# Kernel tuning notes

Measured on AMD Instinct MI355X. Metric: run time of the kernel, lower is better.

## Reference

```python
import jax, jax.numpy as jnp
import numpy as np

EPS = 1e-5

def _layer_norm(x, w, b):
    mu = jnp.mean(x, axis=-1, keepdims=True)
    var = jnp.mean(jnp.square(x - mu), axis=-1, keepdims=True)
    return (x - mu) * jax.lax.rsqrt(var + EPS) * w + b

def setup_inputs() -> dict:
    B, N, C, H, CH = 1, 256, 128, 4, 32
    key = jax.random.key(0)
    ks = jax.random.split(key, 8)
    s = 0.02
    return {
        "z": jax.random.normal(ks[0], (B, N, N, C), dtype=jnp.float32),
        "pair_mask": jnp.ones((B, N, N), dtype=jnp.float32),
        "ln_w": jnp.ones((C,), dtype=jnp.float32),
        "ln_b": jnp.zeros((C,), dtype=jnp.float32),
        "Wq": jax.random.normal(ks[1], (H * CH, C), dtype=jnp.float32) * s,
        "Wk": jax.random.normal(ks[2], (H * CH, C), dtype=jnp.float32) * s,
        "Wv": jax.random.normal(ks[3], (H * CH, C), dtype=jnp.float32) * s,
        "Wb": jax.random.normal(ks[4], (H, C), dtype=jnp.float32) * s,
        "Wg": jax.random.normal(ks[5], (H * CH, C), dtype=jnp.float32) * s,
        "bg": jnp.zeros((H * CH,), dtype=jnp.float32),
        "Wo": jax.random.normal(ks[6], (C, H * CH), dtype=jnp.float32) * s,
        "bo": jnp.zeros((C,), dtype=jnp.float32),
    }

def reference(z, pair_mask, ln_w, ln_b, Wq, Wk, Wv, Wb, Wg, bg, Wo, bo):
    B, I, J, C = z.shape
    H = Wb.shape[0]
    CH = Wq.shape[0] // H
    zn = _layer_norm(z, ln_w, ln_b)                      # (B,I,J,C)
    q = (zn @ Wq.T).reshape(B, I, J, H, CH)
    k = (zn @ Wk.T).reshape(B, I, J, H, CH)
    v = (zn @ Wv.T).reshape(B, I, J, H, CH)
    bias = zn @ Wb.T                                     # (B,I,J,H) -> per-head pair bias
    g = jax.nn.sigmoid(zn @ Wg.T + bg)                   # (B,I,J,H*CH)
    scale = 1.0 / jnp.sqrt(jnp.asarray(CH, z.dtype))
    # logits[b,h,i,j,k] = q_ij . k_ik / sqrt(CH) + bias[b,h,j,k]
    logits = jnp.einsum('bijhd,bikhd->bhijk', q, k) * scale
    logits = logits + jnp.transpose(bias, (0, 3, 1, 2))[:, :, None, :, :]
    # pair mask: (B,i,j,k) outer product, True = attend
    mask2d = (pair_mask[..., :, None] * pair_mask[..., None, :]) > 0.5
    logits = jnp.where(mask2d[:, None], logits, jnp.asarray(-1e9, logits.dtype))
    probs = jax.nn.softmax(logits, axis=-1)
    o = jnp.einsum('bhijk,bikhd->bijhd', probs, v).reshape(B, I, J, H * CH)
    o = g * o
    return o @ Wo.T + bo
```

## Files before the change

### kernel.cpp

```cpp
#include <hip/hip_runtime.h>
#include <hip/hip_bf16.h>

#define ATT_SCALE 0.17677669529663687f
#define LOG2E     1.4426950408889634f

typedef __attribute__((ext_vector_type(8))) short short8v;
typedef __attribute__((ext_vector_type(4))) float f32x4;
typedef __attribute__((ext_vector_type(16))) float f32x16;

__device__ __forceinline__ short f2bf(float f) {
    unsigned u = __builtin_bit_cast(unsigned, f);
    u = u + 0x7fffu + ((u >> 16) & 1u);
    return (short)(u >> 16);
}
__device__ __forceinline__ float bf2f(short s) {
    unsigned u = ((unsigned)(unsigned short)s) << 16;
    return __builtin_bit_cast(float, u);
}
__device__ __forceinline__ unsigned pk2(float lo, float hi) {
    return (unsigned)(unsigned short)f2bf(lo) |
           ((unsigned)(unsigned short)f2bf(hi) << 16);
}
__device__ __forceinline__ float lo16f(unsigned w) {
    return __builtin_bit_cast(float, w << 16);
}
__device__ __forceinline__ float hi16f(unsigned w) {
    return __builtin_bit_cast(float, w & 0xffff0000u);
}
__device__ __forceinline__ float exp2i(float x) {
    float r;
    asm("v_exp_f32 %0, %1" : "=v"(r) : "v"(x));
    return r;
}
__device__ __forceinline__ unsigned short f2h(float f) {
    _Float16 h = (_Float16)f;
    return __builtin_bit_cast(unsigned short, h);
}
__device__ __forceinline__ float h2f(unsigned short u) {
    return (float)__builtin_bit_cast(_Float16, u);
}

__global__ __launch_bounds__(256) void k_wprep(
    const float* __restrict__ Wq, const float* __restrict__ Wk,
    const float* __restrict__ Wv, const float* __restrict__ Wg,
    const float* __restrict__ Wb, const float* __restrict__ Wo,
    unsigned short* __restrict__ wbf, unsigned short* __restrict__ wbbf,
    unsigned short* __restrict__ wohi, unsigned short* __restrict__ wolo)
{
    int idx = blockIdx.x * 256 + threadIdx.x;
    if (idx < 65536) {
        int m = idx >> 14, e = idx & 16383;
        float v;
        if (m == 0)      v = Wq[e] * (ATT_SCALE * LOG2E);
        else if (m == 1) v = Wk[e];
        else if (m == 2) v = Wv[e];
        else             v = Wg[e];
        wbf[idx] = (unsigned short)f2bf(v);
    } else if (idx < 66048) {
        int e = idx - 65536;
        wbbf[e] = (unsigned short)f2bf(Wb[e]);
    } else if (idx < 82432) {
        int e = idx - 66048;
        float w = Wo[e];
        short hv = f2bf(w);
        wohi[e] = (unsigned short)hv;
        wolo[e] = (unsigned short)f2bf(w - bf2f(hv));
    }
}

__global__ __launch_bounds__(256, 4) void k_lnproj(
    const float* __restrict__ z, const float* __restrict__ lnw,
    const float* __restrict__ lnb,
    const unsigned short* __restrict__ wbf, const unsigned short* __restrict__ wbbf,
    const float* __restrict__ bg,
    unsigned short* __restrict__ q_o, unsigned short* __restrict__ k_o,
    unsigned short* __restrict__ vt_o, unsigned short* __restrict__ g_o,
    unsigned* __restrict__ bTP)
{
    __shared__ __align__(16) short zn[64][136];
    __shared__ __align__(16) short wstg[4][32][40];

    const int tid  = threadIdx.x;
    const int lane = tid & 63;
    const int wave = tid >> 6;
    const int l15  = lane & 15;
    const int g    = lane >> 4;
    const int wc   = wave;
    const long p0  = (long)blockIdx.x * 64;
    const int xq   = (int)(p0 >> 8);
    const int y0   = (int)(p0 & 255);

    {
        const int r = tid >> 2, q4 = tid & 3;
        const float* zrow = z + (p0 + r) * 128 + q4 * 32;
        float4 xv[8];
        float s1 = 0.f, s2 = 0.f;
#pragma unroll
        for (int m = 0; m < 8; ++m) {
            xv[m] = *(const float4*)(zrow + m * 4);
            s1 += xv[m].x + xv[m].y + xv[m].z + xv[m].w;
            s2 += xv[m].x * xv[m].x + xv[m].y * xv[m].y +
                  xv[m].z * xv[m].z + xv[m].w * xv[m].w;
        }
        s1 += __shfl_xor(s1, 1); s2 += __shfl_xor(s2, 1);
        s1 += __shfl_xor(s1, 2); s2 += __shfl_xor(s2, 2);
        float mu  = s1 * 0.0078125f;
        float inv = rsqrtf(s2 * 0.0078125f - mu * mu + 1e-5f);
#pragma unroll
        for (int mm = 0; mm < 4; ++mm) {
            float4 a = xv[2 * mm], b = xv[2 * mm + 1];
            const float* wp = lnw + q4 * 32 + mm * 8;
            const float* bp = lnb + q4 * 32 + mm * 8;
            float4 w0 = *(const float4*)wp, w1 = *(const float4*)(wp + 4);
            float4 b0 = *(const float4*)bp, b1 = *(const float4*)(bp + 4);
            uint4 uu;
            uu.x = pk2((a.x - mu) * inv * w0.x + b0.x, (a.y - mu) * inv * w0.y + b0.y);
            uu.y = pk2((a.z - mu) * inv * w0.z + b0.z, (a.w - mu) * inv * w0.w + b0.w);
            uu.z = pk2((b.x - mu) * inv * w1.x + b1.x, (b.y - mu) * inv * w1.y + b1.y);
            uu.w = pk2((b.z - mu) * inv * w1.z + b1.z, (b.w - mu) * inv * w1.w + b1.w);
            *(uint4*)&zn[r][q4 * 32 + mm * 8] = uu;
        }
    }
    __syncthreads();

    if (wc == 0) {
        const unsigned short* wbp = wbbf + (l15 & 3) * 128;
        short8v wb[4];
#pragma unroll
        for (int ks = 0; ks < 4; ++ks)
            wb[ks] = *(const short8v*)(wbp + ks * 32 + g * 8);
        f32x4 bacc[4];
#pragma unroll
        for (int rt = 0; rt < 4; ++rt) bacc[rt] = (f32x4){0.f, 0.f, 0.f, 0.f};
#pragma unroll
        for (int ks = 0; ks < 4; ++ks)
#pragma unroll
            for (int rt = 0; rt < 4; ++rt) {
                short8v a = *(const short8v*)&zn[rt * 16 + l15][ks * 32 + g * 8];
                bacc[rt] = __builtin_amdgcn_mfma_f32_16x16x32_bf16(a, wb[ks], bacc[rt], 0, 0, 0);
            }
        if (l15 < 4) {
#pragma unroll
            for (int rt = 0; rt < 4; ++rt) {
                int kb = y0 + rt * 16 + g * 4;
                unsigned w0 = pk2(bacc[rt][0] * LOG2E, bacc[rt][1] * LOG2E);
                unsigned w1 = pk2(bacc[rt][2] * LOG2E, bacc[rt][3] * LOG2E);
                bTP[l15 * 32768 + (kb >> 1) * 256 + xq]       = w0;
                bTP[l15 * 32768 + ((kb >> 1) + 1) * 256 + xq] = w1;
            }
        }
    }

    for (int wsel = 0; wsel < 4; ++wsel) {
        const unsigned short* __restrict__ W = wbf + wsel * 16384;
        f32x4 acc[4][2];
#pragma unroll
        for (int rt = 0; rt < 4; ++rt) {
            acc[rt][0] = (f32x4){0.f, 0.f, 0.f, 0.f};
            acc[rt][1] = (f32x4){0.f, 0.f, 0.f, 0.f};
        }
#pragma unroll
        for (int ks = 0; ks < 4; ++ks) {
            short8v b0 = *(const short8v*)(W + (wc * 32 + l15) * 128 + ks * 32 + g * 8);
            short8v b1 = *(const short8v*)(W + (wc * 32 + 16 + l15) * 128 + ks * 32 + g * 8);
#pragma unroll
            for (int rt = 0; rt < 4; ++rt) {
                short8v a = *(const short8v*)&zn[rt * 16 + l15][ks * 32 + g * 8];
                acc[rt][0] = __builtin_amdgcn_mfma_f32_16x16x32_bf16(a, b0, acc[rt][0], 0, 0, 0);
                acc[rt][1] = __builtin_amdgcn_mfma_f32_16x16x32_bf16(a, b1, acc[rt][1], 0, 0, 0);
            }
        }

        if (wsel == 3) {
#pragma unroll
            for (int pair = 0; pair < 2; ++pair) {
#pragma unroll
                for (int rt2 = 0; rt2 < 2; ++rt2)
#pragma unroll
                    for (int ct = 0; ct < 2; ++ct) {
                        float bgc = bg[wc * 32 + ct * 16 + l15];
#pragma unroll
                        for (int r = 0; r < 4; ++r) {
                            float val = acc[pair * 2 + rt2][ct][r] + bgc;
                            wstg[wave][rt2 * 16 + g * 4 + r][ct * 16 + l15] =
                                (short)f2h(1.0f / (1.0f + __expf(-val)));
                        }
                    }
#pragma unroll
                for (int ps = 0; ps < 2; ++ps) {
                    int idx = ps * 64 + lane;
                    int lr = idx >> 2, ch = (idx & 3) * 8;
                    short8v vv = *(const short8v*)&wstg[wave][lr][ch];
                    *(short8v*)(g_o + ((long)wc * 65536 + p0 + pair * 32 + lr) * 32 + ch) = vv;
                }
            }
        } else if (wsel == 2) {
#pragma unroll
            for (int pair = 0; pair < 2; ++pair) {
#pragma unroll
                for (int rt2 = 0; rt2 < 2; ++rt2)
#pragma unroll
                    for (int ct = 0; ct < 2; ++ct) {
                        uint2 pw;
                        pw.x = pk2(acc[pair * 2 + rt2][ct][0], acc[pair * 2 + rt2][ct][1]);
                        pw.y = pk2(acc[pair * 2 + rt2][ct][2], acc[pair * 2 + rt2][ct][3]);
                        *(uint2*)&wstg[wave][ct * 16 + l15][rt2 * 16 + g * 4] = pw;
                    }
#pragma unroll
                for (int e = 0; e < 4; ++e) {
                    int idx = e * 64 + lane;
                    int d = idx >> 3, k4 = idx & 7;
                    int k4p = ((k4 & 1) << 1) | ((k4 >> 1) & 1) | (k4 & 4);
                    short4 sv = *(const short4*)&wstg[wave][d][k4 * 4];
                    *(short4*)(vt_o + (((long)wc * 256 + xq) * 32 + d) * 256 +
                               y0 + pair * 32 + k4p * 4) = sv;
                }
            }
        } else {
            unsigned short* __restrict__ O = (wsel == 0) ? q_o : k_o;
#pragma unroll
            for (int pair = 0; pair < 2; ++pair) {
#pragma unroll
                for (int rt2 = 0; rt2 < 2; ++rt2)
#pragma unroll
                    for (int ct = 0; ct < 2; ++ct)
#pragma unroll
                        for (int r = 0; r < 4; ++r)
                            wstg[wave][rt2 * 16 + g * 4 + r][ct * 16 + l15] =
                                f2bf(acc[pair * 2 + rt2][ct][r]);
#pragma unroll
                for (int ps = 0; ps < 2; ++ps) {
                    int idx = ps * 64 + lane;
                    int lr = idx >> 2, ch = (idx & 3) * 8;
                    short8v vv = *(const short8v*)&wstg[wave][lr][ch];
                    *(short8v*)(O + ((long)wc * 65536 + p0 + pair * 32 + lr) * 32 + ch) = vv;
                }
            }
        }
    }
}

__global__ __launch_bounds__(256, 2) void k_attn_mfma(
    const unsigned short* __restrict__ q_ws, const unsigned short* __restrict__ k_ws,
    const unsigned short* __restrict__ vt_ws, const unsigned short* __restrict__ g_ws,
    const unsigned* __restrict__ bTP, const float* __restrict__ pm,
    unsigned short* __restrict__ ob)
{
    __shared__ __align__(16) short Ksh[256][40];
    __shared__ __align__(16) short VTsh[32][264];
    __shared__ float pmsh[256];

    const int tid  = threadIdx.x;
    const int lane = tid & 63;
    const int wave = tid >> 6;
    const int l31  = lane & 31;
    const int hi   = lane >> 5;
    const int bid = blockIdx.x;
    const int xcd = bid & 7, jj = bid >> 3;
    const int h = xcd >> 1;
    const int i = ((xcd & 1) << 7) | jj;
    const long hbase  = ((long)h * 65536 + (long)i * 256) * 32;
    const long vtbase = ((long)h * 256 + i) * 8192;

    pmsh[tid] = pm[i * 256 + tid];
#pragma unroll
    for (int pass = 0; pass < 4; ++pass) {
        int idx = pass * 256 + tid;
        *(short8v*)&Ksh[idx >> 2][(idx & 3) * 8] =
            *(const short8v*)(k_ws + hbase + idx * 8);
        *(short8v*)&VTsh[idx >> 5][(idx & 31) * 8] =
            *(const short8v*)(vt_ws + vtbase + idx * 8);
    }
    __syncthreads();

    bool ok4 = true;
#pragma unroll
    for (int e = 0; e < 4; ++e) ok4 = ok4 && (pmsh[lane * 4 + e] > 0.5f);
    const bool allok = __all(ok4);

    const f32x16 zero16 = {0.f,0.f,0.f,0.f,0.f,0.f,0.f,0.f,
                           0.f,0.f,0.f,0.f,0.f,0.f,0.f,0.f};

    for (int qi = 0; qi < 2; ++qi) {
        const int qb = wave * 2 + qi;
        const int ql = qb * 32 + l31;

        short8v bq0 = *(const short8v*)(q_ws + hbase + (long)ql * 32 + hi * 8);
        short8v bq1 = *(const short8v*)(q_ws + hbase + (long)ql * 32 + 16 + hi * 8);
        const bool rowok = pmsh[ql] > 0.5f;
        const unsigned* btp = bTP + h * 32768 + ql;

        const long grow = hbase + (long)ql * 32;
        ushort4 gu[4];
#pragma unroll
        for (int n = 0; n < 4; ++n)
            gu[n] = *(const ushort4*)(g_ws + grow + n * 8 + hi * 4);

        f32x16 oacc = zero16;
        float ls0 = 0.f, ls1 = 0.f;

        short8v ka0 = *(const short8v*)&Ksh[l31][hi * 8];
        short8v ka1 = *(const short8v*)&Ksh[l31][16 + hi * 8];
        short8v va0 = *(const short8v*)&VTsh[l31][hi * 8];
        short8v va1 = *(const short8v*)&VTsh[l31][16 + hi * 8];
        unsigned bb[8];
#pragma unroll
        for (int n = 0; n < 4; ++n) {
            int m = (n * 8 + hi * 4) >> 1;
            bb[2 * n]     = btp[m * 256];
            bb[2 * n + 1] = btp[(m + 1) * 256];
        }

#pragma unroll
        for (int t = 0; t < 8; ++t) {
            short8v nka0, nka1, nva0, nva1;
            unsigned nbb[8];
            if (t < 7) {
                nka0 = *(const short8v*)&Ksh[(t + 1) * 32 + l31][hi * 8];
                nka1 = *(const short8v*)&Ksh[(t + 1) * 32 + l31][16 + hi * 8];
                nva0 = *(const short8v*)&VTsh[l31][(t + 1) * 32 + hi * 8];
                nva1 = *(const short8v*)&VTsh[l31][(t + 1) * 32 + 16 + hi * 8];
#pragma unroll
                for (int n = 0; n < 4; ++n) {
                    int m = ((t + 1) * 32 + n * 8 + hi * 4) >> 1;
                    nbb[2 * n]     = btp[m * 256];
                    nbb[2 * n + 1] = btp[(m + 1) * 256];
                }
            }

            __builtin_amdgcn_s_setprio(1);
            f32x16 s = __builtin_amdgcn_mfma_f32_32x32x16_bf16(ka0, bq0, zero16, 0, 0, 0);
            s = __builtin_amdgcn_mfma_f32_32x32x16_bf16(ka1, bq1, s, 0, 0, 0);
            __builtin_amdgcn_s_setprio(0);

            uint4 w0, w1;
            if (allok) {
                float p0, p1, p2, p3;
                p0 = exp2i(s[0] + lo16f(bb[0])); p1 = exp2i(s[1] + hi16f(bb[0]));
                p2 = exp2i(s[2] + lo16f(bb[1])); p3 = exp2i(s[3] + hi16f(bb[1]));
                ls0 += (p0 + p1) + (p2 + p3);
                w0.x = pk2(p0, p1); w0.y = pk2(p2, p3);
                p0 = exp2i(s[4] + lo16f(bb[2])); p1 = exp2i(s[5] + hi16f(bb[2]));
                p2 = exp2i(s[6] + lo16f(bb[3])); p3 = exp2i(s[7] + hi16f(bb[3]));
                ls1 += (p0 + p1) + (p2 + p3);
                w0.z = pk2(p0, p1); w0.w = pk2(p2, p3);
                p0 = exp2i(s[8] + lo16f(bb[4])); p1 = exp2i(s[9] + hi16f(bb[4]));
                p2 = exp2i(s[10] + lo16f(bb[5])); p3 = exp2i(s[11] + hi16f(bb[5]));
                ls0 += (p0 + p1) + (p2 + p3);
                w1.x = pk2(p0, p1); w1.y = pk2(p2, p3);
                p0 = exp2i(s[12] + lo16f(bb[6])); p1 = exp2i(s[13] + hi16f(bb[6]));
                p2 = exp2i(s[14] + lo16f(bb[7])); p3 = exp2i(s[15] + hi16f(bb[7]));
                ls1 += (p0 + p1) + (p2 + p3);
                w1.z = pk2(p0, p1); w1.w = pk2(p2, p3);
            } else {
#pragma unroll
                for (int n = 0; n < 4; ++n) {
                    f32x4 ma = *(const f32x4*)&pmsh[t * 32 + n * 8 + hi * 4];
                    float p0 = exp2i(rowok ? s[4*n+0] + lo16f(bb[2*n])   + ((ma[0] > 0.5f) ? 0.f : -1e9f) : 0.0f);
                    float p1 = exp2i(rowok ? s[4*n+1] + hi16f(bb[2*n])   + ((ma[1] > 0.5f) ? 0.f : -1e9f) : 0.0f);
                    float p2 = exp2i(rowok ? s[4*n+2] + lo16f(bb[2*n+1]) + ((ma[2] > 0.5f) ? 0.f : -1e9f) : 0.0f);
                    float p3 = exp2i(rowok ? s[4*n+3] + hi16f(bb[2*n+1]) + ((ma[3] > 0.5f) ? 0.f : -1e9f) : 0.0f);
                    ls0 += (p0 + p1) + (p2 + p3);
                    unsigned wa = pk2(p0, p1), wb = pk2(p2, p3);
                    if (n == 0) { w0.x = wa; w0.y = wb; }
                    else if (n == 1) { w0.z = wa; w0.w = wb; }
                    else if (n == 2) { w1.x = wa; w1.y = wb; }
                    else { w1.z = wa; w1.w = wb; }
                }
            }
            short8v pb0 = *(short8v*)&w0;
            short8v pb1 = *(short8v*)&w1;

            __builtin_amdgcn_s_setprio(1);
            oacc = __builtin_amdgcn_mfma_f32_32x32x16_bf16(va0, pb0, oacc, 0, 0, 0);
            oacc = __builtin_amdgcn_mfma_f32_32x32x16_bf16(va1, pb1, oacc, 0, 0, 0);
            __builtin_amdgcn_s_setprio(0);

            if (t < 7) {
                ka0 = nka0; ka1 = nka1; va0 = nva0; va1 = nva1;
#pragma unroll
                for (int e = 0; e < 8; ++e) bb[e] = nbb[e];
            }
        }

        float lsum = ls0 + ls1;
        lsum += __shfl_xor(lsum, 32);
        const float linv = 1.0f / lsum;

        const long orow = (long)(i * 256 + ql) * 128 + h * 32;
#pragma unroll
        for (int n = 0; n < 4; ++n) {
            int dbase = n * 8 + hi * 4;
            float v0 = oacc[4 * n + 0] * linv * h2f(gu[n].x);
            float v1 = oacc[4 * n + 1] * linv * h2f(gu[n].y);
            float v2 = oacc[4 * n + 2] * linv * h2f(gu[n].z);
            float v3 = oacc[4 * n + 3] * linv * h2f(gu[n].w);
            short4 sh = {f2bf(v0), f2bf(v1), f2bf(v2), f2bf(v3)};
            *(short4*)(ob + orow + dbase) = sh;
        }
    }
}

__global__ __launch_bounds__(256, 4) void k_outproj(
    const unsigned short* __restrict__ ob,
    const unsigned short* __restrict__ wohi, const unsigned short* __restrict__ wolo,
    const float* __restrict__ bo, float* __restrict__ out)
{
    const int tid  = threadIdx.x;
    const int lane = tid & 63;
    const int wave = tid >> 6;
    const int l15  = lane & 15;
    const int g    = lane >> 4;
    const int wc   = wave;
    const long p0  = (long)blockIdx.x * 64;

    f32x4 acc[4][2];
#pragma unroll
    for (int rt = 0; rt < 4; ++rt) {
        acc[rt][0] = (f32x4){0.f, 0.f, 0.f, 0.f};
        acc[rt][1] = (f32x4){0.f, 0.f, 0.f, 0.f};
    }

#pragma unroll
    for (int ks = 0; ks < 4; ++ks) {
        const int wof = ks * 32 + g * 8;
        short8v bh0 = *(const short8v*)(wohi + (wc * 32 + l15) * 128 + wof);
        short8v bh1 = *(const short8v*)(wohi + (wc * 32 + 16 + l15) * 128 + wof);
        short8v bl0 = *(const short8v*)(wolo + (wc * 32 + l15) * 128 + wof);
        short8v bl1 = *(const short8v*)(wolo + (wc * 32 + 16 + l15) * 128 + wof);
#pragma unroll
        for (int rt = 0; rt < 4; ++rt) {
            long aoff = (p0 + rt * 16 + l15) * 128 + ks * 32 + g * 8;
            short8v ah = *(const short8v*)(ob + aoff);
            acc[rt][0] = __builtin_amdgcn_mfma_f32_16x16x32_bf16(ah, bh0, acc[rt][0], 0, 0, 0);
            acc[rt][0] = __builtin_amdgcn_mfma_f32_16x16x32_bf16(ah, bl0, acc[rt][0], 0, 0, 0);
            acc[rt][1] = __builtin_amdgcn_mfma_f32_16x16x32_bf16(ah, bh1, acc[rt][1], 0, 0, 0);
            acc[rt][1] = __builtin_amdgcn_mfma_f32_16x16x32_bf16(ah, bl1, acc[rt][1], 0, 0, 0);
        }
    }

#pragma unroll
    for (int ct = 0; ct < 2; ++ct) {
        float bv = bo[wc * 32 + ct * 16 + l15];
#pragma unroll
        for (int rt = 0; rt < 4; ++rt)
#pragma unroll
            for (int r = 0; r < 4; ++r)
                out[(p0 + rt * 16 + g * 4 + r) * 128 +
                    wc * 32 + ct * 16 + l15] = acc[rt][ct][r] + bv;
    }
}

extern "C" void kernel_launch(void* const* d_in, const int* in_sizes, int n_in,
                              void* d_out, int out_size, void* d_ws, size_t ws_size,
                              hipStream_t stream) {
    const float* z   = (const float*)d_in[0];
    const float* pm  = (const float*)d_in[1];
    const float* lnw = (const float*)d_in[2];
    const float* lnb = (const float*)d_in[3];
    const float* Wq  = (const float*)d_in[4];
    const float* Wk  = (const float*)d_in[5];
    const float* Wv  = (const float*)d_in[6];
    const float* Wb  = (const float*)d_in[7];
    const float* Wg  = (const float*)d_in[8];
    const float* bg  = (const float*)d_in[9];
    const float* Wo  = (const float*)d_in[10];
    const float* bo  = (const float*)d_in[11];
    float* out = (float*)d_out;

    unsigned short* wsS  = (unsigned short*)d_ws;
    unsigned short* wbf  = wsS;
    unsigned short* wbbf = wsS + 65536;
    unsigned short* wohi = wsS + 66048;
    unsigned short* wolo = wsS + 82432;
    unsigned* bTP        = (unsigned*)(wsS + 98816);
    unsigned short* qb   = wsS + 360960;
    unsigned short* kb   = qb + 8388608;
    unsigned short* vtb  = kb + 8388608;
    unsigned short* obw  = vtb + 8388608;
    unsigned short* ghw  = obw + 8388608;

    k_wprep<<<322, 256, 0, stream>>>(Wq, Wk, Wv, Wg, Wb, Wo, wbf, wbbf, wohi, wolo);
    k_lnproj<<<1024, 256, 0, stream>>>(z, lnw, lnb, wbf, wbbf, bg, qb, kb, vtb, ghw, bTP);
    k_attn_mfma<<<1024, 256, 0, stream>>>(qb, kb, vtb, ghw, bTP, pm, obw);
    k_outproj<<<1024, 256, 0, stream>>>(obw, wohi, wolo, bo, out);
}
```

Baseline: 92.68 us.

## Fuse attention with output projection per row and use nontemporal stores

```diff
diff --git a/kernel.cpp b/kernel.cpp
--- a/kernel.cpp
+++ b/kernel.cpp
@@ -7,6 +7,7 @@
 typedef __attribute__((ext_vector_type(8))) short short8v;
 typedef __attribute__((ext_vector_type(4))) float f32x4;
 typedef __attribute__((ext_vector_type(16))) float f32x16;
+typedef __attribute__((ext_vector_type(2))) unsigned uint2v;
 
 __device__ __forceinline__ short f2bf(float f) {
     unsigned u = __builtin_bit_cast(unsigned, f);
@@ -191,7 +192,8 @@
                     int idx = ps * 64 + lane;
                     int lr = idx >> 2, ch = (idx & 3) * 8;
                     short8v vv = *(const short8v*)&wstg[wave][lr][ch];
-                    *(short8v*)(g_o + ((long)wc * 65536 + p0 + pair * 32 + lr) * 32 + ch) = vv;
+                    __builtin_nontemporal_store(vv,
+                        (short8v*)(g_o + ((long)wc * 65536 + p0 + pair * 32 + lr) * 32 + ch));
                 }
             }
         } else if (wsel == 2) {
@@ -211,9 +213,10 @@
                     int idx = e * 64 + lane;
                     int d = idx >> 3, k4 = idx & 7;
                     int k4p = ((k4 & 1) << 1) | ((k4 >> 1) & 1) | (k4 & 4);
-                    short4 sv = *(const short4*)&wstg[wave][d][k4 * 4];
-                    *(short4*)(vt_o + (((long)wc * 256 + xq) * 32 + d) * 256 +
-                               y0 + pair * 32 + k4p * 4) = sv;
+                    uint2v sv = *(const uint2v*)&wstg[wave][d][k4 * 4];
+                    __builtin_nontemporal_store(sv,
+                        (uint2v*)(vt_o + (((long)wc * 256 + xq) * 32 + d) * 256 +
+                                  y0 + pair * 32 + k4p * 4));
                 }
             }
         } else {
@@ -233,43 +236,48 @@
                     int idx = ps * 64 + lane;
                     int lr = idx >> 2, ch = (idx & 3) * 8;
                     short8v vv = *(const short8v*)&wstg[wave][lr][ch];
-                    *(short8v*)(O + ((long)wc * 65536 + p0 + pair * 32 + lr) * 32 + ch) = vv;
+                    __builtin_nontemporal_store(vv,
+                        (short8v*)(O + ((long)wc * 65536 + p0 + pair * 32 + lr) * 32 + ch));
                 }
             }
         }
     }
 }
 
-__global__ __launch_bounds__(256, 2) void k_attn_mfma(
+__global__ __launch_bounds__(512, 2) void k_attn_out(
     const unsigned short* __restrict__ q_ws, const unsigned short* __restrict__ k_ws,
     const unsigned short* __restrict__ vt_ws, const unsigned short* __restrict__ g_ws,
     const unsigned* __restrict__ bTP, const float* __restrict__ pm,
-    unsigned short* __restrict__ ob)
+    const unsigned short* __restrict__ wohi, const unsigned short* __restrict__ wolo,
+    const float* __restrict__ bo, float* __restrict__ out)
 {
-    __shared__ __align__(16) short Ksh[256][40];
-    __shared__ __align__(16) short VTsh[32][264];
-    __shared__ float pmsh[256];
+    __shared__ __align__(16) char smem[150528];
+    short* smS = (short*)smem;
+#define KSH(h,r,c)  smS[(h) * 10240 + (r) * 40 + (c)]
+#define VTSH(h,d,c) smS[40960 + (h) * 8448 + (d) * 264 + (c)]
+#define OLDS(r,c)   smS[40960 + (r) * 132 + (c)]
+    float* pmsh = (float*)(smem + 149504);
 
     const int tid  = threadIdx.x;
     const int lane = tid & 63;
     const int wave = tid >> 6;
     const int l31  = lane & 31;
     const int hi   = lane >> 5;
-    const int bid = blockIdx.x;
-    const int xcd = bid & 7, jj = bid >> 3;
-    const int h = xcd >> 1;
-    const int i = ((xcd & 1) << 7) | jj;
-    const long hbase  = ((long)h * 65536 + (long)i * 256) * 32;
-    const long vtbase = ((long)h * 256 + i) * 8192;
-
-    pmsh[tid] = pm[i * 256 + tid];
-#pragma unroll
-    for (int pass = 0; pass < 4; ++pass) {
-        int idx = pass * 256 + tid;
-        *(short8v*)&Ksh[idx >> 2][(idx & 3) * 8] =
-            *(const short8v*)(k_ws + hbase + idx * 8);
-        *(short8v*)&VTsh[idx >> 5][(idx & 31) * 8] =
-            *(const short8v*)(vt_ws + vtbase + idx * 8);
+    const int h    = wave >> 1;
+    const int qh   = wave & 1;
+    const int i    = blockIdx.x;
+
+    if (tid < 256) pmsh[tid] = pm[i * 256 + tid];
+#pragma unroll
+    for (int pass = 0; pass < 8; ++pass) {
+        int idx = pass * 512 + tid;
+        int hh = idx >> 10, rem = idx & 1023;
+        *(short8v*)&KSH(hh, rem >> 2, (rem & 3) * 8) =
+            *(const short8v*)(k_ws + ((long)hh * 65536 + i * 256 + (rem >> 2)) * 32 +
+                              (rem & 3) * 8);
+        *(short8v*)&VTSH(hh, rem >> 5, (rem & 31) * 8) =
+            *(const short8v*)(vt_ws + ((long)hh * 256 + i) * 8192 +
+                              (rem >> 5) * 256 + (rem & 31) * 8);
     }
     __syncthreads();
 
@@ -280,9 +288,13 @@
 
     const f32x16 zero16 = {0.f,0.f,0.f,0.f,0.f,0.f,0.f,0.f,
                            0.f,0.f,0.f,0.f,0.f,0.f,0.f,0.f};
-
-    for (int qi = 0; qi < 2; ++qi) {
-        const int qb = wave * 2 + qi;
+    const long hbase = ((long)h * 65536 + (long)i * 256) * 32;
+
+    unsigned opk[4][8];
+
+#pragma unroll
+    for (int qi = 0; qi < 4; ++qi) {
+        const int qb = qh * 4 + qi;
         const int ql = qb * 32 + l31;
 
         short8v bq0 = *(const short8v*)(q_ws + hbase + (long)ql * 32 + hi * 8);
@@ -299,10 +311,10 @@
         f32x16 oacc = zero16;
         float ls0 = 0.f, ls1 = 0.f;
 
-        short8v ka0 = *(const short8v*)&Ksh[l31][hi * 8];
-        short8v ka1 = *(const short8v*)&Ksh[l31][16 + hi * 8];
-        short8v va0 = *(const short8v*)&VTsh[l31][hi * 8];
-        short8v va1 = *(const short8v*)&VTsh[l31][16 + hi * 8];
+        short8v ka0 = *(const short8v*)&KSH(h, l31, hi * 8);
+        short8v ka1 = *(const short8v*)&KSH(h, l31, 16 + hi * 8);
+        short8v va0 = *(const short8v*)&VTSH(h, l31, hi * 8);
+        short8v va1 = *(const short8v*)&VTSH(h, l31, 16 + hi * 8);
         unsigned bb[8];
 #pragma unroll
         for (int n = 0; n < 4; ++n) {
@@ -316,10 +328,10 @@
             short8v nka0, nka1, nva0, nva1;
             unsigned nbb[8];
             if (t < 7) {
-                nka0 = *(const short8v*)&Ksh[(t + 1) * 32 + l31][hi * 8];
-                nka1 = *(const short8v*)&Ksh[(t + 1) * 32 + l31][16 + hi * 8];
-                nva0 = *(const short8v*)&VTsh[l31][(t + 1) * 32 + hi * 8];
-                nva1 = *(const short8v*)&VTsh[l31][(t + 1) * 32 + 16 + hi * 8];
+                nka0 = *(const short8v*)&KSH(h, (t + 1) * 32 + l31, hi * 8);
+                nka1 = *(const short8v*)&KSH(h, (t + 1) * 32 + l31, 16 + hi * 8);
+                nva0 = *(const short8v*)&VTSH(h, l31, (t + 1) * 32 + hi * 8);
+                nva1 = *(const short8v*)&VTSH(h, l31, (t + 1) * 32 + 16 + hi * 8);
 #pragma unroll
                 for (int n = 0; n < 4; ++n) {
                     int m = ((t + 1) * 32 + n * 8 + hi * 4) >> 1;
@@ -387,68 +399,74 @@
         lsum += __shfl_xor(lsum, 32);
         const float linv = 1.0f / lsum;
 
-        const long orow = (long)(i * 256 + ql) * 128 + h * 32;
 #pragma unroll
         for (int n = 0; n < 4; ++n) {
-            int dbase = n * 8 + hi * 4;
             float v0 = oacc[4 * n + 0] * linv * h2f(gu[n].x);
             float v1 = oacc[4 * n + 1] * linv * h2f(gu[n].y);
             float v2 = oacc[4 * n + 2] * linv * h2f(gu[n].z);
             float v3 = oacc[4 * n + 3] * linv * h2f(gu[n].w);
-            short4 sh = {f2bf(v0), f2bf(v1), f2bf(v2), f2bf(v3)};
-            *(short4*)(ob + orow + dbase) = sh;
-        }
-    }
-}
-
-__global__ __launch_bounds__(256, 4) void k_outproj(
-    const unsigned short* __restrict__ ob,
-    const unsigned short* __restrict__ wohi, const unsigned short* __restrict__ wolo,
-    const float* __restrict__ bo, float* __restrict__ out)
-{
-    const int tid  = threadIdx.x;
-    const int lane = tid & 63;
-    const int wave = tid >> 6;
-    const int l15  = lane & 15;
-    const int g    = lane >> 4;
-    const int wc   = wave;
-    const long p0  = (long)blockIdx.x * 64;
-
-    f32x4 acc[4][2];
-#pragma unroll
-    for (int rt = 0; rt < 4; ++rt) {
-        acc[rt][0] = (f32x4){0.f, 0.f, 0.f, 0.f};
-        acc[rt][1] = (f32x4){0.f, 0.f, 0.f, 0.f};
-    }
-
-#pragma unroll
-    for (int ks = 0; ks < 4; ++ks) {
-        const int wof = ks * 32 + g * 8;
-        short8v bh0 = *(const short8v*)(wohi + (wc * 32 + l15) * 128 + wof);
-        short8v bh1 = *(const short8v*)(wohi + (wc * 32 + 16 + l15) * 128 + wof);
-        short8v bl0 = *(const short8v*)(wolo + (wc * 32 + l15) * 128 + wof);
-        short8v bl1 = *(const short8v*)(wolo + (wc * 32 + 16 + l15) * 128 + wof);
-#pragma unroll
-        for (int rt = 0; rt < 4; ++rt) {
-            long aoff = (p0 + rt * 16 + l15) * 128 + ks * 32 + g * 8;
-            short8v ah = *(const short8v*)(ob + aoff);
-            acc[rt][0] = __builtin_amdgcn_mfma_f32_16x16x32_bf16(ah, bh0, acc[rt][0], 0, 0, 0);
-            acc[rt][0] = __builtin_amdgcn_mfma_f32_16x16x32_bf16(ah, bl0, acc[rt][0], 0, 0, 0);
-            acc[rt][1] = __builtin_amdgcn_mfma_f32_16x16x32_bf16(ah, bh1, acc[rt][1], 0, 0, 0);
-            acc[rt][1] = __builtin_amdgcn_mfma_f32_16x16x32_bf16(ah, bl1, acc[rt][1], 0, 0, 0);
-        }
-    }
-
-#pragma unroll
-    for (int ct = 0; ct < 2; ++ct) {
-        float bv = bo[wc * 32 + ct * 16 + l15];
-#pragma unroll
-        for (int rt = 0; rt < 4; ++rt)
-#pragma unroll
-            for (int r = 0; r < 4; ++r)
-                out[(p0 + rt * 16 + g * 4 + r) * 128 +
-                    wc * 32 + ct * 16 + l15] = acc[rt][ct][r] + bv;
-    }
+            opk[qi][2 * n]     = pk2(v0, v1);
+            opk[qi][2 * n + 1] = pk2(v2, v3);
+        }
+    }
+
+    __syncthreads();
+#pragma unroll
+    for (int qi = 0; qi < 4; ++qi) {
+        const int ql = (qh * 4 + qi) * 32 + l31;
+#pragma unroll
+        for (int n = 0; n < 4; ++n) {
+            uint2 w;
+            w.x = opk[qi][2 * n];
+            w.y = opk[qi][2 * n + 1];
+            *(uint2*)&OLDS(ql, h * 32 + n * 8 + hi * 4) = w;
+        }
+    }
+    __syncthreads();
+
+    {
+        const int l15 = lane & 15;
+        const int g4  = lane >> 4;
+        const int r0  = wave * 32;
+
+        f32x4 acc[2][8];
+#pragma unroll
+        for (int rt = 0; rt < 2; ++rt)
+#pragma unroll
+            for (int ct = 0; ct < 8; ++ct)
+                acc[rt][ct] = (f32x4){0.f, 0.f, 0.f, 0.f};
+
+#pragma unroll
+        for (int ks = 0; ks < 4; ++ks) {
+            short8v ah0 = *(const short8v*)&OLDS(r0 + l15, ks * 32 + g4 * 8);
+            short8v ah1 = *(const short8v*)&OLDS(r0 + 16 + l15, ks * 32 + g4 * 8);
+#pragma unroll
+            for (int ct = 0; ct < 8; ++ct) {
+                const int wof = (ct * 16 + l15) * 128 + ks * 32 + g4 * 8;
+                short8v bh = *(const short8v*)(wohi + wof);
+                short8v bl = *(const short8v*)(wolo + wof);
+                acc[0][ct] = __builtin_amdgcn_mfma_f32_16x16x32_bf16(ah0, bh, acc[0][ct], 0, 0, 0);
+                acc[0][ct] = __builtin_amdgcn_mfma_f32_16x16x32_bf16(ah0, bl, acc[0][ct], 0, 0, 0);
+                acc[1][ct] = __builtin_amdgcn_mfma_f32_16x16x32_bf16(ah1, bh, acc[1][ct], 0, 0, 0);
+                acc[1][ct] = __builtin_amdgcn_mfma_f32_16x16x32_bf16(ah1, bl, acc[1][ct], 0, 0, 0);
+            }
+        }
+
+#pragma unroll
+        for (int ct = 0; ct < 8; ++ct) {
+            float bv = bo[ct * 16 + l15];
+#pragma unroll
+            for (int rt = 0; rt < 2; ++rt)
+#pragma unroll
+                for (int r = 0; r < 4; ++r)
+                    __builtin_nontemporal_store(acc[rt][ct][r] + bv,
+                        out + ((long)i * 256 + r0 + rt * 16 + g4 * 4 + r) * 128 +
+                        ct * 16 + l15);
+        }
+    }
+#undef KSH
+#undef VTSH
+#undef OLDS
 }
 
 extern "C" void kernel_launch(void* const* d_in, const int* in_sizes, int n_in,
@@ -477,11 +495,9 @@
     unsigned short* qb   = wsS + 360960;
     unsigned short* kb   = qb + 8388608;
     unsigned short* vtb  = kb + 8388608;
-    unsigned short* obw  = vtb + 8388608;
-    unsigned short* ghw  = obw + 8388608;
+    unsigned short* ghw  = vtb + 8388608;
 
     k_wprep<<<322, 256, 0, stream>>>(Wq, Wk, Wv, Wg, Wb, Wo, wbf, wbbf, wohi, wolo);
     k_lnproj<<<1024, 256, 0, stream>>>(z, lnw, lnb, wbf, wbbf, bg, qb, kb, vtb, ghw, bTP);
-    k_attn_mfma<<<1024, 256, 0, stream>>>(qb, kb, vtb, ghw, bTP, pm, obw);
-    k_outproj<<<1024, 256, 0, stream>>>(obw, wohi, wolo, bo, out);
-}
+    k_attn_out<<<256, 512, 0, stream>>>(qb, kb, vtb, ghw, bTP, pm, wohi, wolo, bo, out);
+}
```

Result: slower. 102.1 us (+10.2%).
